# Optimization experiments

Measured on AMD Instinct MI355X. Metric: run time of the kernel, lower is better.

## Reference

```python
import jax, jax.numpy as jnp
import numpy as np

N_NODES = 50000
D = 64            # encoder.out_node_dim
N_EDGES = 800000
HID = 64          # mlp_edge_model_dim


def setup_inputs() -> dict:
    key = jax.random.key(0)
    k1, k2, k3, k4 = jax.random.split(key, 4)
    node_emb = jax.random.normal(k1, (N_NODES, D), dtype=jnp.float32)
    edge_index = jax.random.randint(k2, (2, N_EDGES), 0, N_NODES, dtype=jnp.int64)
    # Xavier-uniform style init for the 2-layer edge MLP
    lim1 = np.sqrt(6.0 / (2 * D + HID)).astype(np.float32)
    lim2 = np.sqrt(6.0 / (HID + 1)).astype(np.float32)
    W1 = jax.random.uniform(k3, (2 * D, HID), minval=-lim1, maxval=lim1, dtype=jnp.float32)
    b1 = jnp.zeros((HID,), dtype=jnp.float32)
    W2 = jax.random.uniform(k4, (HID, 1), minval=-lim2, maxval=lim2, dtype=jnp.float32)
    b2 = jnp.zeros((1,), dtype=jnp.float32)
    return {"node_emb": node_emb, "edge_index": edge_index,
            "W1": W1, "b1": b1, "W2": W2, "b2": b2}


def reference(node_emb, edge_index, W1, b1, W2, b2):
    src, dst = edge_index[0], edge_index[1]
    emb_src = node_emb[src]              # [E, D] gather
    emb_dst = node_emb[dst]              # [E, D] gather
    edge_emb = jnp.concatenate([emb_src, emb_dst], axis=1)  # [E, 2D]
    h = jax.nn.relu(edge_emb @ W1 + b1)  # [E, HID]
    edge_logits = h @ W2 + b2            # [E, 1]
    return edge_logits
```

## Files before the change

### kernel.cpp

```cpp
#include <hip/hip_runtime.h>


typedef __attribute__((ext_vector_type(8))) short short8;
typedef __attribute__((ext_vector_type(4))) float f32x4;

__device__ __forceinline__ unsigned short f2bf_rne(float f) {
    union { float f; unsigned u; } v;
    v.f = f;
    return (unsigned short)((v.u + 0x7FFFu + ((v.u >> 16) & 1u)) >> 16);
}

__global__ void cvt_to_bf16(const float* __restrict__ x,
                            unsigned short* __restrict__ y, int n4) {
    int i = blockIdx.x * blockDim.x + threadIdx.x;
    if (i >= n4) return;
    f32x4 v = ((const f32x4*)x)[i];
    ushort4 o;
    o.x = f2bf_rne(v[0]);
    o.y = f2bf_rne(v[1]);
    o.z = f2bf_rne(v[2]);
    o.w = f2bf_rne(v[3]);
    ((ushort4*)y)[i] = o;
}

#define W1T_STRIDE 136

__global__ void edge_mlp(const int* __restrict__ eidx,
                         const unsigned short* __restrict__ nodebf,
                         const float* __restrict__ W1,
                         const float* __restrict__ b1,
                         const float* __restrict__ W2,
                         const float* __restrict__ b2,
                         float* __restrict__ out,
                         int E, int ntiles) {
    __shared__ __align__(16) unsigned short w1t[64 * W1T_STRIDE];

    const int tid = threadIdx.x;

#pragma unroll
    for (int i = 0; i < 32; ++i) {
        int idx = tid + i * 256;
        int k = idx >> 6;
        int n = idx & 63;
        w1t[n * W1T_STRIDE + k] = f2bf_rne(W1[idx]);
    }
    __syncthreads();

    const int lane = tid & 63;
    const int wid = tid >> 6;
    const int c = lane & 15;
    const int quad = lane >> 4;

    short8 bfrag[4][4];
#pragma unroll
    for (int nt = 0; nt < 4; ++nt)
#pragma unroll
        for (int kc = 0; kc < 4; ++kc) {
            const short8* p =
                (const short8*)&w1t[(nt * 16 + c) * W1T_STRIDE + kc * 32 + quad * 8];
            bfrag[nt][kc] = *p;
        }

    float w2v[4], b1v[4];
#pragma unroll
    for (int nt = 0; nt < 4; ++nt) {
        w2v[nt] = W2[nt * 16 + c];
        b1v[nt] = b1[nt * 16 + c];
    }
    const float b2v = b2[0];

    const int wave_global = blockIdx.x * 4 + wid;
    const int wave_stride = gridDim.x * 4;
    const int ko = quad * 8;

    for (int t = wave_global; t < ntiles; t += wave_stride) {
        int e = t * 16 + c;
        int ec = (e < E) ? e : (E - 1);
        int src = eidx[ec];
        int dst = eidx[E + ec];

        const unsigned short* rs = nodebf + (size_t)src * 64;
        const unsigned short* rd = nodebf + (size_t)dst * 64;
        short8 a0 = *(const short8*)(rs + ko);
        short8 a1 = *(const short8*)(rs + 32 + ko);
        short8 a2 = *(const short8*)(rd + ko);
        short8 a3 = *(const short8*)(rd + 32 + ko);

        f32x4 acc[4];
#pragma unroll
        for (int nt = 0; nt < 4; ++nt) acc[nt] = (f32x4){0.f, 0.f, 0.f, 0.f};

#pragma unroll
        for (int nt = 0; nt < 4; ++nt) {
            acc[nt] = __builtin_amdgcn_mfma_f32_16x16x32_bf16(a0, bfrag[nt][0], acc[nt], 0, 0, 0);
            acc[nt] = __builtin_amdgcn_mfma_f32_16x16x32_bf16(a1, bfrag[nt][1], acc[nt], 0, 0, 0);
            acc[nt] = __builtin_amdgcn_mfma_f32_16x16x32_bf16(a2, bfrag[nt][2], acc[nt], 0, 0, 0);
            acc[nt] = __builtin_amdgcn_mfma_f32_16x16x32_bf16(a3, bfrag[nt][3], acc[nt], 0, 0, 0);
        }

        float p[4];
#pragma unroll
        for (int r = 0; r < 4; ++r) p[r] = 0.f;
#pragma unroll
        for (int nt = 0; nt < 4; ++nt) {
#pragma unroll
            for (int r = 0; r < 4; ++r) {
                float h = acc[nt][r] + b1v[nt];
                h = fmaxf(h, 0.f);
                p[r] += h * w2v[nt];
            }
        }
#pragma unroll
        for (int m = 1; m < 16; m <<= 1) {
#pragma unroll
            for (int r = 0; r < 4; ++r) p[r] += __shfl_xor(p[r], m, 16);
        }

        if (c == 0) {
            int base = t * 16 + quad * 4;
            if (base + 3 < E) {
                f32x4 o = {p[0] + b2v, p[1] + b2v, p[2] + b2v, p[3] + b2v};
                *(f32x4*)(out + base) = o;
            } else {
#pragma unroll
                for (int r = 0; r < 4; ++r)
                    if (base + r < E) out[base + r] = p[r] + b2v;
            }
        }
    }
}

extern "C" void kernel_launch(void* const* d_in, const int* in_sizes, int n_in,
                              void* d_out, int out_size, void* d_ws, size_t ws_size,
                              hipStream_t stream) {
    const float* node = (const float*)d_in[0];
    const int* eidx = (const int*)d_in[1];
    const float* W1 = (const float*)d_in[2];
    const float* b1 = (const float*)d_in[3];
    const float* W2 = (const float*)d_in[4];
    const float* b2 = (const float*)d_in[5];
    float* out = (float*)d_out;

    const int node_elems = in_sizes[0];
    const int E = in_sizes[1] / 2;
    const int n4 = node_elems / 4;

    unsigned short* nodebf = (unsigned short*)d_ws;

    cvt_to_bf16<<<(n4 + 255) / 256, 256, 0, stream>>>(node, nodebf, n4);

    const int ntiles = (E + 15) / 16;
    edge_mlp<<<1024, 256, 0, stream>>>(eidx, nodebf, W1, b1, W2, b2, out, E, ntiles);
}
```

Baseline: 104.9 us.

## Software-pipeline edge index and row gathers across tiles, double grid size

The tile loop becomes a software pipeline: the node rows for the next tile and the edge indices for the tile after that are loaded while the current tile's MFMAs and reduction run. The grid grows from 1024 to 2048 blocks, and launch bounds request 3 blocks per CU so register allocation stays bounded. The aim is to hide the dependent gather latency (index load, then row load) behind compute. The cost is more live registers per wave, and each wave now handles fewer tiles, so the pipeline has less room to pay off.

```diff
diff --git a/kernel.cpp b/kernel.cpp
--- a/kernel.cpp
+++ b/kernel.cpp
@@ -25,14 +25,29 @@
 
 #define W1T_STRIDE 136
 
-__global__ void edge_mlp(const int* __restrict__ eidx,
-                         const unsigned short* __restrict__ nodebf,
-                         const float* __restrict__ W1,
-                         const float* __restrict__ b1,
-                         const float* __restrict__ W2,
-                         const float* __restrict__ b2,
-                         float* __restrict__ out,
-                         int E, int ntiles) {
+struct Rows { short8 a0, a1, a2, a3; };
+
+__device__ __forceinline__ Rows load_rows(const unsigned short* __restrict__ nodebf,
+                                          int src, int dst, int ko) {
+    Rows r;
+    const unsigned short* rs = nodebf + (size_t)src * 64;
+    const unsigned short* rd = nodebf + (size_t)dst * 64;
+    r.a0 = *(const short8*)(rs + ko);
+    r.a1 = *(const short8*)(rs + 32 + ko);
+    r.a2 = *(const short8*)(rd + ko);
+    r.a3 = *(const short8*)(rd + 32 + ko);
+    return r;
+}
+
+__global__ __launch_bounds__(256, 3)
+void edge_mlp(const int* __restrict__ eidx,
+              const unsigned short* __restrict__ nodebf,
+              const float* __restrict__ W1,
+              const float* __restrict__ b1,
+              const float* __restrict__ W2,
+              const float* __restrict__ b2,
+              float* __restrict__ out,
+              int E, int ntiles) {
     __shared__ __align__(16) unsigned short w1t[64 * W1T_STRIDE];
 
     const int tid = threadIdx.x;
@@ -50,16 +65,15 @@
     const int wid = tid >> 6;
     const int c = lane & 15;
     const int quad = lane >> 4;
+    const int ko = quad * 8;
 
     short8 bfrag[4][4];
 #pragma unroll
     for (int nt = 0; nt < 4; ++nt)
 #pragma unroll
-        for (int kc = 0; kc < 4; ++kc) {
-            const short8* p =
-                (const short8*)&w1t[(nt * 16 + c) * W1T_STRIDE + kc * 32 + quad * 8];
-            bfrag[nt][kc] = *p;
-        }
+        for (int kc = 0; kc < 4; ++kc)
+            bfrag[nt][kc] =
+                *(const short8*)&w1t[(nt * 16 + c) * W1T_STRIDE + kc * 32 + quad * 8];
 
     float w2v[4], b1v[4];
 #pragma unroll
@@ -69,52 +83,64 @@
     }
     const float b2v = b2[0];
 
-    const int wave_global = blockIdx.x * 4 + wid;
-    const int wave_stride = gridDim.x * 4;
-    const int ko = quad * 8;
+    const int stride = gridDim.x * 4;
+    int t = blockIdx.x * 4 + wid;
+    int tn = t + stride;
 
-    for (int t = wave_global; t < ntiles; t += wave_stride) {
+    int snxt = 0, dnxt = 0;
+    Rows cur;
+    if (t < ntiles) {
         int e = t * 16 + c;
         int ec = (e < E) ? e : (E - 1);
-        int src = eidx[ec];
-        int dst = eidx[E + ec];
+        int s = eidx[ec], d = eidx[E + ec];
+        cur = load_rows(nodebf, s, d, ko);
+        if (tn < ntiles) {
+            int en = tn * 16 + c;
+            int enc = (en < E) ? en : (E - 1);
+            snxt = eidx[enc];
+            dnxt = eidx[E + enc];
+        }
+    }
 
-        const unsigned short* rs = nodebf + (size_t)src * 64;
-        const unsigned short* rd = nodebf + (size_t)dst * 64;
-        short8 a0 = *(const short8*)(rs + ko);
-        short8 a1 = *(const short8*)(rs + 32 + ko);
-        short8 a2 = *(const short8*)(rd + ko);
-        short8 a3 = *(const short8*)(rd + 32 + ko);
+    for (; t < ntiles; t += stride, tn += stride) {
+        const bool has_next = (tn < ntiles);
+        Rows nxt;
+        if (has_next) nxt = load_rows(nodebf, snxt, dnxt, ko);
+
+        int t2 = tn + stride;
+        int s2 = 0, d2 = 0;
+        if (t2 < ntiles) {
+            int e2 = t2 * 16 + c;
+            int e2c = (e2 < E) ? e2 : (E - 1);
+            s2 = eidx[e2c];
+            d2 = eidx[E + e2c];
+        }
 
         f32x4 acc[4];
 #pragma unroll
         for (int nt = 0; nt < 4; ++nt) acc[nt] = (f32x4){0.f, 0.f, 0.f, 0.f};
-
 #pragma unroll
         for (int nt = 0; nt < 4; ++nt) {
-            acc[nt] = __builtin_amdgcn_mfma_f32_16x16x32_bf16(a0, bfrag[nt][0], acc[nt], 0, 0, 0);
-            acc[nt] = __builtin_amdgcn_mfma_f32_16x16x32_bf16(a1, bfrag[nt][1], acc[nt], 0, 0, 0);
-            acc[nt] = __builtin_amdgcn_mfma_f32_16x16x32_bf16(a2, bfrag[nt][2], acc[nt], 0, 0, 0);
-            acc[nt] = __builtin_amdgcn_mfma_f32_16x16x32_bf16(a3, bfrag[nt][3], acc[nt], 0, 0, 0);
+            acc[nt] = __builtin_amdgcn_mfma_f32_16x16x32_bf16(cur.a0, bfrag[nt][0], acc[nt], 0, 0, 0);
+            acc[nt] = __builtin_amdgcn_mfma_f32_16x16x32_bf16(cur.a1, bfrag[nt][1], acc[nt], 0, 0, 0);
+            acc[nt] = __builtin_amdgcn_mfma_f32_16x16x32_bf16(cur.a2, bfrag[nt][2], acc[nt], 0, 0, 0);
+            acc[nt] = __builtin_amdgcn_mfma_f32_16x16x32_bf16(cur.a3, bfrag[nt][3], acc[nt], 0, 0, 0);
         }
 
         float p[4];
 #pragma unroll
         for (int r = 0; r < 4; ++r) p[r] = 0.f;
 #pragma unroll
-        for (int nt = 0; nt < 4; ++nt) {
+        for (int nt = 0; nt < 4; ++nt)
 #pragma unroll
             for (int r = 0; r < 4; ++r) {
-                float h = acc[nt][r] + b1v[nt];
-                h = fmaxf(h, 0.f);
-                p[r] += h * w2v[nt];
+                float h = fmaxf(acc[nt][r] + b1v[nt], 0.f);
+                p[r] = fmaf(h, w2v[nt], p[r]);
             }
-        }
 #pragma unroll
-        for (int m = 1; m < 16; m <<= 1) {
+        for (int m = 1; m < 16; m <<= 1)
 #pragma unroll
             for (int r = 0; r < 4; ++r) p[r] += __shfl_xor(p[r], m, 16);
-        }
 
         if (c == 0) {
             int base = t * 16 + quad * 4;
@@ -127,6 +153,10 @@
                     if (base + r < E) out[base + r] = p[r] + b2v;
             }
         }
+
+        if (has_next) cur = nxt;
+        snxt = s2;
+        dnxt = d2;
     }
 }
 
@@ -150,5 +180,5 @@
     cvt_to_bf16<<<(n4 + 255) / 256, 256, 0, stream>>>(node, nodebf, n4);
 
     const int ntiles = (E + 15) / 16;
-    edge_mlp<<<1024, 256, 0, stream>>>(eidx, nodebf, W1, b1, W2, b2, out, E, ntiles);
+    edge_mlp<<<2048, 256, 0, stream>>>(eidx, nodebf, W1, b1, W2, b2, out, E, ntiles);
 }
```

Result: slower. 113.8 us (+8.6%).

## Precompute per-node first-layer projections and reduce edge MLP to gather-add

Applied to the files above, without the earlier changes.

The first linear layer is split across the concatenation, so each node's contributions W1_src·x and W1_dst·x are computed once per node with MFMA and stored as fp16 in a workspace. The edge kernel then gathers two 64-wide fp16 vectors per edge, adds them, applies ReLU and dots with W2, with 8 threads per edge reducing via shuffles. This removes the per-edge matmul, whose work scales with 800k edges, in exchange for a 50k-node matmul and fp16 rounding of the pre-activations.

```diff
diff --git a/kernel.cpp b/kernel.cpp
--- a/kernel.cpp
+++ b/kernel.cpp
@@ -3,6 +3,7 @@
 
 typedef __attribute__((ext_vector_type(8))) short short8;
 typedef __attribute__((ext_vector_type(4))) float f32x4;
+typedef __attribute__((ext_vector_type(8))) _Float16 half8;
 
 __device__ __forceinline__ unsigned short f2bf_rne(float f) {
     union { float f; unsigned u; } v;
@@ -10,39 +11,27 @@
     return (unsigned short)((v.u + 0x7FFFu + ((v.u >> 16) & 1u)) >> 16);
 }
 
-__global__ void cvt_to_bf16(const float* __restrict__ x,
-                            unsigned short* __restrict__ y, int n4) {
-    int i = blockIdx.x * blockDim.x + threadIdx.x;
-    if (i >= n4) return;
-    f32x4 v = ((const f32x4*)x)[i];
-    ushort4 o;
-    o.x = f2bf_rne(v[0]);
-    o.y = f2bf_rne(v[1]);
-    o.z = f2bf_rne(v[2]);
-    o.w = f2bf_rne(v[3]);
-    ((ushort4*)y)[i] = o;
-}
+#define W1T_K 72
+#define CT_STRIDE 136
 
-#define W1T_STRIDE 136
-
-__global__ void edge_mlp(const int* __restrict__ eidx,
-                         const unsigned short* __restrict__ nodebf,
-                         const float* __restrict__ W1,
-                         const float* __restrict__ b1,
-                         const float* __restrict__ W2,
-                         const float* __restrict__ b2,
-                         float* __restrict__ out,
-                         int E, int ntiles) {
-    __shared__ __align__(16) unsigned short w1t[64 * W1T_STRIDE];
+__global__ __launch_bounds__(256)
+void node_uv(const float* __restrict__ X,
+             const float* __restrict__ W1,
+             const float* __restrict__ b1,
+             _Float16* __restrict__ UV,
+             int nnodes, int ntiles) {
+    __shared__ __align__(16) unsigned short w1t[128 * W1T_K];
+    __shared__ __align__(16) _Float16 cbuf[4][16 * CT_STRIDE];
 
     const int tid = threadIdx.x;
-
 #pragma unroll
     for (int i = 0; i < 32; ++i) {
         int idx = tid + i * 256;
-        int k = idx >> 6;
-        int n = idx & 63;
-        w1t[n * W1T_STRIDE + k] = f2bf_rne(W1[idx]);
+        int r = idx >> 6;
+        int col = idx & 63;
+        int k = r & 63;
+        int jp = col + (r & 64);
+        w1t[jp * W1T_K + k] = f2bf_rne(W1[idx]);
     }
     __syncthreads();
 
@@ -51,89 +40,103 @@
     const int c = lane & 15;
     const int quad = lane >> 4;
 
-    short8 bfrag[4][4];
+    const int t = blockIdx.x * 4 + wid;
+    if (t >= ntiles) return;
+
+    short8 bfrag[8][2];
 #pragma unroll
-    for (int nt = 0; nt < 4; ++nt)
+    for (int nt = 0; nt < 8; ++nt)
 #pragma unroll
-        for (int kc = 0; kc < 4; ++kc) {
-            const short8* p =
-                (const short8*)&w1t[(nt * 16 + c) * W1T_STRIDE + kc * 32 + quad * 8];
-            bfrag[nt][kc] = *p;
-        }
+        for (int kc = 0; kc < 2; ++kc)
+            bfrag[nt][kc] =
+                *(const short8*)&w1t[(nt * 16 + c) * W1T_K + kc * 32 + quad * 8];
 
-    float w2v[4], b1v[4];
+    float b1v[8];
 #pragma unroll
-    for (int nt = 0; nt < 4; ++nt) {
-        w2v[nt] = W2[nt * 16 + c];
-        b1v[nt] = b1[nt * 16 + c];
+    for (int nt = 0; nt < 8; ++nt)
+        b1v[nt] = (nt < 4) ? b1[nt * 16 + c] : 0.f;
+
+    int n = t * 16 + c;
+    n = (n < nnodes) ? n : (nnodes - 1);
+    const float* xr = X + (size_t)n * 64 + quad * 8;
+    f32x4 x0a = *(const f32x4*)(xr);
+    f32x4 x0b = *(const f32x4*)(xr + 4);
+    f32x4 x1a = *(const f32x4*)(xr + 32);
+    f32x4 x1b = *(const f32x4*)(xr + 36);
+    short8 a0, a1;
+#pragma unroll
+    for (int i = 0; i < 4; ++i) {
+        a0[i] = (short)f2bf_rne(x0a[i]);
+        a0[4 + i] = (short)f2bf_rne(x0b[i]);
+        a1[i] = (short)f2bf_rne(x1a[i]);
+        a1[4 + i] = (short)f2bf_rne(x1b[i]);
     }
-    const float b2v = b2[0];
 
-    const int wave_global = blockIdx.x * 4 + wid;
-    const int wave_stride = gridDim.x * 4;
-    const int ko = quad * 8;
+    f32x4 acc[8];
+#pragma unroll
+    for (int nt = 0; nt < 8; ++nt) acc[nt] = (f32x4){0.f, 0.f, 0.f, 0.f};
+#pragma unroll
+    for (int nt = 0; nt < 8; ++nt) {
+        acc[nt] = __builtin_amdgcn_mfma_f32_16x16x32_bf16(a0, bfrag[nt][0], acc[nt], 0, 0, 0);
+        acc[nt] = __builtin_amdgcn_mfma_f32_16x16x32_bf16(a1, bfrag[nt][1], acc[nt], 0, 0, 0);
+    }
 
-    for (int t = wave_global; t < ntiles; t += wave_stride) {
-        int e = t * 16 + c;
-        int ec = (e < E) ? e : (E - 1);
-        int src = eidx[ec];
-        int dst = eidx[E + ec];
+    _Float16* cb = cbuf[wid];
+#pragma unroll
+    for (int nt = 0; nt < 8; ++nt)
+#pragma unroll
+        for (int r = 0; r < 4; ++r)
+            cb[(quad * 4 + r) * CT_STRIDE + nt * 16 + c] =
+                (_Float16)(acc[nt][r] + b1v[nt]);
 
-        const unsigned short* rs = nodebf + (size_t)src * 64;
-        const unsigned short* rd = nodebf + (size_t)dst * 64;
-        short8 a0 = *(const short8*)(rs + ko);
-        short8 a1 = *(const short8*)(rs + 32 + ko);
-        short8 a2 = *(const short8*)(rd + ko);
-        short8 a3 = *(const short8*)(rd + 32 + ko);
+    __builtin_amdgcn_s_waitcnt(0);
 
-        f32x4 acc[4];
+    const _Float16* rp = &cb[(lane >> 2) * CT_STRIDE + (lane & 3) * 32];
+    const f32x4* s4 = (const f32x4*)rp;
+    f32x4* dst = (f32x4*)(UV + (size_t)t * 2048 + lane * 32);
+    dst[0] = s4[0];
+    dst[1] = s4[1];
+    dst[2] = s4[2];
+    dst[3] = s4[3];
+}
+
+__global__ __launch_bounds__(256)
+void edge_out(const int* __restrict__ eidx,
+              const _Float16* __restrict__ UV,
+              const float* __restrict__ W2,
+              const float* __restrict__ b2,
+              float* __restrict__ out, int E) {
+    int tid = blockIdx.x * 256 + threadIdx.x;
+    int e = tid >> 3;
+    int j = tid & 7;
+    if (e >= E) return;
+
+    int src = eidx[e];
+    int dst = eidx[E + e];
+
+    half8 u = *(const half8*)(UV + (size_t)src * 128 + j * 8);
+    half8 v = *(const half8*)(UV + (size_t)dst * 128 + 64 + j * 8);
+    f32x4 w2a = *(const f32x4*)(W2 + j * 8);
+    f32x4 w2b = *(const f32x4*)(W2 + j * 8 + 4);
+
+    float acc = 0.f;
 #pragma unroll
-        for (int nt = 0; nt < 4; ++nt) acc[nt] = (f32x4){0.f, 0.f, 0.f, 0.f};
-
-#pragma unroll
-        for (int nt = 0; nt < 4; ++nt) {
-            acc[nt] = __builtin_amdgcn_mfma_f32_16x16x32_bf16(a0, bfrag[nt][0], acc[nt], 0, 0, 0);
-            acc[nt] = __builtin_amdgcn_mfma_f32_16x16x32_bf16(a1, bfrag[nt][1], acc[nt], 0, 0, 0);
-            acc[nt] = __builtin_amdgcn_mfma_f32_16x16x32_bf16(a2, bfrag[nt][2], acc[nt], 0, 0, 0);
-            acc[nt] = __builtin_amdgcn_mfma_f32_16x16x32_bf16(a3, bfrag[nt][3], acc[nt], 0, 0, 0);
-        }
-
-        float p[4];
-#pragma unroll
-        for (int r = 0; r < 4; ++r) p[r] = 0.f;
-#pragma unroll
-        for (int nt = 0; nt < 4; ++nt) {
-#pragma unroll
-            for (int r = 0; r < 4; ++r) {
-                float h = acc[nt][r] + b1v[nt];
-                h = fmaxf(h, 0.f);
-                p[r] += h * w2v[nt];
-            }
-        }
-#pragma unroll
-        for (int m = 1; m < 16; m <<= 1) {
-#pragma unroll
-            for (int r = 0; r < 4; ++r) p[r] += __shfl_xor(p[r], m, 16);
-        }
-
-        if (c == 0) {
-            int base = t * 16 + quad * 4;
-            if (base + 3 < E) {
-                f32x4 o = {p[0] + b2v, p[1] + b2v, p[2] + b2v, p[3] + b2v};
-                *(f32x4*)(out + base) = o;
-            } else {
-#pragma unroll
-                for (int r = 0; r < 4; ++r)
-                    if (base + r < E) out[base + r] = p[r] + b2v;
-            }
-        }
+    for (int i = 0; i < 4; ++i) {
+        float h0 = fmaxf((float)u[i] + (float)v[i], 0.f);
+        float h1 = fmaxf((float)u[4 + i] + (float)v[4 + i], 0.f);
+        acc = fmaf(h0, w2a[i], acc);
+        acc = fmaf(h1, w2b[i], acc);
     }
+    acc += __shfl_xor(acc, 1, 8);
+    acc += __shfl_xor(acc, 2, 8);
+    acc += __shfl_xor(acc, 4, 8);
+    if (j == 0) out[e] = acc + b2[0];
 }
 
 extern "C" void kernel_launch(void* const* d_in, const int* in_sizes, int n_in,
                               void* d_out, int out_size, void* d_ws, size_t ws_size,
                               hipStream_t stream) {
-    const float* node = (const float*)d_in[0];
+    const float* X = (const float*)d_in[0];
     const int* eidx = (const int*)d_in[1];
     const float* W1 = (const float*)d_in[2];
     const float* b1 = (const float*)d_in[3];
@@ -141,14 +144,14 @@
     const float* b2 = (const float*)d_in[5];
     float* out = (float*)d_out;
 
-    const int node_elems = in_sizes[0];
+    const int nnodes = in_sizes[0] / 64;
     const int E = in_sizes[1] / 2;
-    const int n4 = node_elems / 4;
 
-    unsigned short* nodebf = (unsigned short*)d_ws;
+    _Float16* UV = (_Float16*)d_ws;
 
-    cvt_to_bf16<<<(n4 + 255) / 256, 256, 0, stream>>>(node, nodebf, n4);
+    const int ntiles = (nnodes + 15) / 16;
+    node_uv<<<(ntiles + 3) / 4, 256, 0, stream>>>(X, W1, b1, UV, nnodes, ntiles);
 
-    const int ntiles = (E + 15) / 16;
-    edge_mlp<<<1024, 256, 0, stream>>>(eidx, nodebf, W1, b1, W2, b2, out, E, ntiles);
+    const int nthreads = E * 8;
+    edge_out<<<(nthreads + 255) / 256, 256, 0, stream>>>(eidx, UV, W2, b2, out, E);
 }
```

After: 103.1 us. Within noise of the previous version (-1.6%).
